# Performance work log

Hardware: AMD Instinct MI355X
Metric: run time of the kernel (lower is better)

The kernel has to match this reference:

```python
import jax, jax.numpy as jnp
import numpy as np

NEG = -1e30  # safe 'log zero' for fp32 (avoids -inf NaNs in grads)


def _ctc_loss(logits, targets, input_lengths, target_lengths):
    """PyTorch-semantics CTC loss: blank=0, reduction='mean', zero_infinity=True.
    logits: [B,T,C] (pre-log-softmax), targets: [B,S] padded, lengths: [B].
    """
    B, T, C = logits.shape
    S = targets.shape[1]
    L = 2 * S + 1  # extended target length (blanks interleaved)
    logp = jax.nn.log_softmax(logits, axis=-1)  # [B,T,C]

    # extended targets: blank, y1, blank, y2, ..., blank
    ext = jnp.zeros((B, L), jnp.int32).at[:, 1::2].set(targets.astype(jnp.int32))
    lp_ext = jnp.take_along_axis(
        logp, jnp.broadcast_to(ext[:, None, :], (B, T, L)), axis=2)  # [B,T,L]

    pos = jnp.arange(L)
    ext_m2 = jnp.pad(ext, ((0, 0), (2, 0)))[:, :L]
    can_skip = (ext != 0) & (ext != ext_m2) & (pos >= 2)  # [B,L]

    def shift(a, k):
        return jnp.pad(a, ((0, 0), (k, 0)), constant_values=NEG)[:, :L]

    def lse3(a, b, c):
        m = jnp.maximum(jnp.maximum(a, b), c)
        return m + jnp.log(jnp.exp(a - m) + jnp.exp(b - m) + jnp.exp(c - m))

    alpha0 = (jnp.full((B, L), NEG, logits.dtype)
              .at[:, 0].set(lp_ext[:, 0, 0])
              .at[:, 1].set(lp_ext[:, 0, 1]))

    def step(alpha, xs):
        lp_t, t = xs  # lp_t: [B,L]
        a2 = shift(alpha, 1)
        a3 = jnp.where(can_skip, shift(alpha, 2), NEG)
        new = lp_t + lse3(alpha, a2, a3)
        # freeze alpha once past each sample's input_length
        alpha = jnp.where((t < input_lengths)[:, None], new, alpha)
        return alpha, None

    lp_T = jnp.swapaxes(lp_ext, 0, 1)  # [T,B,L]
    alpha, _ = jax.lax.scan(step, alpha0, (lp_T[1:], jnp.arange(1, T)))

    i1 = (2 * target_lengths - 1).astype(jnp.int32)
    i2 = (2 * target_lengths).astype(jnp.int32)
    a_last = jnp.take_along_axis(alpha, i1[:, None], axis=1)[:, 0]
    a_blank = jnp.take_along_axis(alpha, i2[:, None], axis=1)[:, 0]
    loss = -jnp.logaddexp(a_last, a_blank)  # [B]
    loss = jnp.where(loss > 1e29, 0.0, loss)  # zero_infinity=True
    return jnp.mean(loss / target_lengths.astype(loss.dtype))


def setup_inputs() -> dict:
    key = jax.random.key(0)
    ks = jax.random.split(key, 8)
    B, T = 32, 2000
    C_err, S_err = 4, 50
    C_ph, S_ph = 64, 200
    error_logits = jax.random.normal(ks[0], (B, T, C_err), jnp.float32)
    phoneme_logits = jax.random.normal(ks[1], (B, T, C_ph), jnp.float32)
    # labels in [1, C): blank=0 never appears in targets
    error_targets = jax.random.randint(ks[2], (B, S_err), 1, C_err, jnp.int32)
    phoneme_targets = jax.random.randint(ks[3], (B, S_ph), 1, C_ph, jnp.int32)
    error_input_lengths = jax.random.randint(ks[4], (B,), T - T // 4, T + 1, jnp.int32)
    phoneme_input_lengths = jax.random.randint(ks[5], (B,), T - T // 4, T + 1, jnp.int32)
    error_target_lengths = jax.random.randint(ks[6], (B,), S_err // 2, S_err + 1, jnp.int32)
    phoneme_target_lengths = jax.random.randint(ks[7], (B,), S_ph // 2, S_ph + 1, jnp.int32)
    return {
        "error_logits": error_logits,
        "phoneme_logits": phoneme_logits,
        "error_targets": error_targets,
        "phoneme_targets": phoneme_targets,
        "error_input_lengths": error_input_lengths,
        "phoneme_input_lengths": phoneme_input_lengths,
        "error_target_lengths": error_target_lengths,
        "phoneme_target_lengths": phoneme_target_lengths,
    }


def reference(error_logits, phoneme_logits, error_targets, phoneme_targets,
              error_input_lengths, phoneme_input_lengths,
              error_target_lengths, phoneme_target_lengths):
    error_weight = 1.0
    phoneme_weight = 1.0
    error_loss = _ctc_loss(error_logits, error_targets,
                           error_input_lengths, error_target_lengths)
    phoneme_loss = _ctc_loss(phoneme_logits, phoneme_targets,
                             phoneme_input_lengths, phoneme_target_lengths)
    total_loss = error_weight * error_loss + phoneme_weight * phoneme_loss
    return total_loss
```

## Files before the change

kernel.cpp:

```cpp
#include <hip/hip_runtime.h>
#include <math.h>


static constexpr float  LOG2E = 1.4426950408889634f;
static constexpr double LN2D  = 0.6931471805599453;
static constexpr int GROWS = 2032;

#define DPP_WAVE_SHL1   0x130
#define DPP_WAVE_SHR1   0x138
#define DPP_ROW_SHR(n)  (0x110 | (n))
#define DPP_ROW_BCAST15 0x142
#define DPP_ROW_BCAST31 0x143

__device__ __forceinline__ float fexp2(float x) {
  return __builtin_amdgcn_exp2f(x);
}
__device__ __forceinline__ float flog2(float x) {
  return __builtin_amdgcn_logf(x);
}

__device__ __forceinline__ double dpp_shr1_f64(double x) {
  int lo = __double2loint(x), hi = __double2hiint(x);
  lo = __builtin_amdgcn_update_dpp(0, lo, DPP_WAVE_SHR1, 0xf, 0xf, true);
  hi = __builtin_amdgcn_update_dpp(0, hi, DPP_WAVE_SHR1, 0xf, 0xf, true);
  return __hiloint2double(hi, lo);
}

__device__ __forceinline__ double dpp_shl1_f64(double x) {
  int lo = __double2loint(x), hi = __double2hiint(x);
  lo = __builtin_amdgcn_update_dpp(0, lo, DPP_WAVE_SHL1, 0xf, 0xf, true);
  hi = __builtin_amdgcn_update_dpp(0, hi, DPP_WAVE_SHL1, 0xf, 0xf, true);
  return __hiloint2double(hi, lo);
}

__device__ __forceinline__ int imax2(int a, int b) { return a > b ? a : b; }

__device__ __forceinline__ int wave_imax(int v) {
  v = imax2(v, __builtin_amdgcn_update_dpp(0, v, DPP_ROW_SHR(1), 0xf, 0xf, true));
  v = imax2(v, __builtin_amdgcn_update_dpp(0, v, DPP_ROW_SHR(2), 0xf, 0xf, true));
  v = imax2(v, __builtin_amdgcn_update_dpp(0, v, DPP_ROW_SHR(4), 0xf, 0xf, true));
  v = imax2(v, __builtin_amdgcn_update_dpp(0, v, DPP_ROW_SHR(8), 0xf, 0xf, true));
  v = imax2(v, __builtin_amdgcn_update_dpp(0, v, DPP_ROW_BCAST15, 0xf, 0xf, true));
  v = imax2(v, __builtin_amdgcn_update_dpp(0, v, DPP_ROW_BCAST31, 0xf, 0xf, true));
  return __builtin_amdgcn_readlane(v, 63);
}


__global__ __launch_bounds__(256) void gather_ph_kernel(
    const float* __restrict__ ph_logits, const float* __restrict__ err_logits,
    const int* __restrict__ ph_tgt,
    float* __restrict__ Gph, float* __restrict__ Lpb_ph,
    float* __restrict__ Lpb_er, float* __restrict__ out) {
  const int bx = blockIdx.x, b = blockIdx.y;
  const int tid = threadIdx.x;
  const int lane = tid & 63, wv = tid >> 6;

  if (bx == 0 && b == 0 && tid == 0) *out = 0.f;

  if (wv == 0 && lane < 32) {
    const int t = bx * 32 + lane;
    if (t < 2000) {
      const float4 v = *(const float4*)(err_logits + ((size_t)b * 2000 + t) * 4);
      const float z0 = v.x * LOG2E;
      const float s = fexp2(z0) + fexp2(v.y * LOG2E) + fexp2(v.z * LOG2E) +
                      fexp2(v.w * LOG2E);
      Lpb_er[(size_t)b * GROWS + t] = z0 - flog2(s);
    }
  }

  const int* tb = ph_tgt + b * 200;
  int idx[4];
  float msk[4];
#pragma unroll
  for (int k = 0; k < 4; ++k) {
    const int si = lane * 4 + k;
    const int cls = (si < 200) ? tb[si] : 0;
    idx[k] = cls << 2;
    msk[k] = (si < 200) ? 1.0f : 0.0f;
  }
  const int t0 = (bx * 4 + wv) * 8;
  float z[8], e[8], s[8];
#pragma unroll
  for (int u = 0; u < 8; ++u) {
    const int t = t0 + u;
    const int tc = (t < 2000) ? t : 1999;
    z[u] = ph_logits[((size_t)b * 2000 + tc) * 64 + lane] * LOG2E;
    e[u] = fexp2(z[u]);
    s[u] = e[u];
  }
#pragma unroll
  for (int off = 32; off >= 1; off >>= 1) {
#pragma unroll
    for (int u = 0; u < 8; ++u) s[u] += __shfl_xor(s[u], off, 64);
  }
#pragma unroll
  for (int u = 0; u < 8; ++u) {
    const int t = t0 + u;
    if (t < 2000) {
      const float e0 = __int_as_float(
          __builtin_amdgcn_readlane(__float_as_int(e[u]), 0));
      const float inv0 = 1.0f / e0;
      float o[4];
#pragma unroll
      for (int k = 0; k < 4; ++k) {
        const float v = __int_as_float(
            __builtin_amdgcn_ds_bpermute(idx[k], __float_as_int(e[u])));
        o[k] = msk[k] * v * inv0;
      }
      *(float4*)(Gph + ((size_t)b * GROWS + t) * 256 + lane * 4) =
          make_float4(o[0], o[1], o[2], o[3]);
      if (lane == 0)
        Lpb_ph[(size_t)b * GROWS + t] = z[u] - flog2(s[u]);
    }
  }
}

template <int P> struct RowP { float v[P]; };

template <int P>
__device__ __forceinline__ void bl_renorm(double (&B)[P], double (&L)[P],
                                          int& K, int tgt) {
  double mm = B[0];
#pragma unroll
  for (int k = 0; k < P; ++k) mm = fmax(fmax(mm, B[k]), L[k]);
  const int ex = (__double2hiint(mm) >> 20) & 0x7ff;
  const int emax = wave_imax(ex);
  if (emax > 0) {
    int d = tgt - emax;
    if (d > 1023) d = 1023;
    if (d < -1022) d = -1022;
    const double sc = __hiloint2double((d + 1023) << 20, 0);
#pragma unroll
    for (int k = 0; k < P; ++k) { B[k] *= sc; L[k] *= sc; }
    K += d;
  }
}

template <int P>
__device__ __forceinline__ void bl_step(double (&B)[P], double (&L)[P],
                                        const double (&skipm)[P],
                                        const RowP<P>& f) {
  const double Lm1 = dpp_shr1_f64(L[P - 1]);
  double nB[P], nL[P];
#pragma unroll
  for (int k = 0; k < P; ++k) {
    const double Lp = (k >= 1) ? L[k - 1] : Lm1;
    nB[k] = B[k] + Lp;
    nL[k] = (double)f.v[k] * fma(skipm[k], Lp, B[k] + L[k]);
  }
#pragma unroll
  for (int k = 0; k < P; ++k) { B[k] = nB[k]; L[k] = nL[k]; }
}

template <int P>
__device__ __forceinline__ void bl_step_bwd(double (&B)[P], double (&L)[P],
                                            const double (&sknext)[P],
                                            const RowP<P>& f) {
  double w[P];
#pragma unroll
  for (int k = 0; k < P; ++k) w[k] = (double)f.v[k] * L[k];
  const double wN = dpp_shl1_f64(w[0]);
  const double BN = dpp_shl1_f64(B[0]);
  double nB[P], nL[P];
#pragma unroll
  for (int k = 0; k < P; ++k) {
    const double wp1 = (k < P - 1) ? w[k + 1] : wN;
    const double Bp1 = (k < P - 1) ? B[k + 1] : BN;
    nB[k] = B[k] + w[k];
    nL[k] = fma(sknext[k], wp1, w[k] + Bp1);
  }
#pragma unroll
  for (int k = 0; k < P; ++k) { B[k] = nB[k]; L[k] = nL[k]; }
}

__device__ __forceinline__ float spb_sum(const float* __restrict__ Lpb,
                                         int len, int lane) {
  float spb = 0.f;
  for (int t0 = lane; t0 < len; t0 += 512) {
#pragma unroll
    for (int u = 0; u < 8; ++u) {
      const int t = t0 + u * 64;
      const int tc = (t < len) ? t : 0;
      const float v = Lpb[tc];
      spb += (t < len) ? v : 0.0f;
    }
  }
#pragma unroll
  for (int off = 32; off >= 1; off >>= 1) spb += __shfl_xor(spb, off, 64);
  return spb;
}

template <int P, typename LdF, typename UseF>
__device__ __forceinline__ void run_fwd(int nsteps, LdF ldrow, UseF use,
                                        double (&B)[P], double (&L)[P],
                                        const double (&sk)[P], int& K) {
  using Buf = decltype(ldrow(1));
  const int ng = nsteps / 16;
  Buf bufA[16], bufB[16];
  if (ng >= 1) {
#pragma unroll
    for (int u = 0; u < 16; ++u) bufA[u] = ldrow(1 + u);
  }
  if (ng >= 2) {
#pragma unroll
    for (int u = 0; u < 16; ++u) bufB[u] = ldrow(17 + u);
  }
  int g = 0;
  for (; g + 2 <= ng; g += 2) {
    bl_renorm<P>(B, L, K, 1523);
    {
      const int gn = (g + 2 < ng) ? (g + 2) : 0;
#pragma unroll
      for (int u = 0; u < 16; ++u) {
        bl_step<P>(B, L, sk, use(bufA[u]));
        bufA[u] = ldrow(1 + gn * 16 + u);
      }
    }
    bl_renorm<P>(B, L, K, 1523);
    {
      const int gn = (g + 3 < ng) ? (g + 3) : 0;
#pragma unroll
      for (int u = 0; u < 16; ++u) {
        bl_step<P>(B, L, sk, use(bufB[u]));
        bufB[u] = ldrow(1 + gn * 16 + u);
      }
    }
  }
  if (g < ng) {
    bl_renorm<P>(B, L, K, 1523);
#pragma unroll
    for (int u = 0; u < 16; ++u) bl_step<P>(B, L, sk, use(bufA[u]));
    ++g;
  }
  {
    const int tstart = 1 + ng * 16;
    Buf bufT[15];
#pragma unroll
    for (int u = 0; u < 15; ++u) {
      int t = tstart + u;
      if (t > nsteps) t = (nsteps > 0) ? nsteps : 1;
      bufT[u] = ldrow(t);
    }
#pragma unroll
    for (int u = 0; u < 15; ++u) {
      if (tstart + u <= nsteps) {
        if (u == 0) bl_renorm<P>(B, L, K, 1523);
        bl_step<P>(B, L, sk, use(bufT[u]));
      }
    }
  }
}

template <int P, typename LdF, typename UseF>
__device__ __forceinline__ void run_bwd(int len, int M, LdF ldrow, UseF use,
                                        double (&B)[P], double (&L)[P],
                                        const double (&sk)[P], int& K) {
  using Buf = decltype(ldrow(1));
  const int ng = M / 16;
  Buf bufA[16], bufB[16];
  if (ng >= 1) {
#pragma unroll
    for (int u = 0; u < 16; ++u) bufA[u] = ldrow(len - 1 - u);
  }
  if (ng >= 2) {
#pragma unroll
    for (int u = 0; u < 16; ++u) bufB[u] = ldrow(len - 17 - u);
  }
  int g = 0;
  for (; g + 2 <= ng; g += 2) {
    bl_renorm<P>(B, L, K, 1023);
    {
      const int jb = (g + 2 < ng) ? (g + 2) * 16 : 0;
#pragma unroll
      for (int u = 0; u < 16; ++u) {
        bl_step_bwd<P>(B, L, sk, use(bufA[u]));
        bufA[u] = ldrow(len - 1 - jb - u);
      }
    }
    bl_renorm<P>(B, L, K, 1023);
    {
      const int jb = (g + 3 < ng) ? (g + 3) * 16 : 0;
#pragma unroll
      for (int u = 0; u < 16; ++u) {
        bl_step_bwd<P>(B, L, sk, use(bufB[u]));
        bufB[u] = ldrow(len - 1 - jb - u);
      }
    }
  }
  if (g < ng) {
    bl_renorm<P>(B, L, K, 1023);
#pragma unroll
    for (int u = 0; u < 16; ++u) bl_step_bwd<P>(B, L, sk, use(bufA[u]));
    ++g;
  }
  {
    const int jstart = ng * 16;
    Buf bufT[15];
#pragma unroll
    for (int u = 0; u < 15; ++u) {
      int j = jstart + u;
      if (j > M - 1) j = (M > 0) ? (M - 1) : 0;
      bufT[u] = ldrow(len - 1 - j);
    }
#pragma unroll
    for (int u = 0; u < 15; ++u) {
      if (jstart + u < M) {
        if (u == 0) bl_renorm<P>(B, L, K, 1023);
        bl_step_bwd<P>(B, L, sk, use(bufT[u]));
      }
    }
  }
}

__global__ __launch_bounds__(64) void ctc_half_kernel(
    const float* __restrict__ Gph, const float* __restrict__ err_logits,
    const int* __restrict__ ph_tgt, const int* __restrict__ err_tgt,
    const int* __restrict__ err_il, const int* __restrict__ ph_il,
    const int* __restrict__ err_tl, const int* __restrict__ ph_tl,
    const float* __restrict__ Lpb_ph, const float* __restrict__ Lpb_er,
    double* __restrict__ st, int* __restrict__ Ks,
    float* __restrict__ spbA) {
  const int blk = blockIdx.x;
  const int dir = blk >> 6;
  const int c = blk & 63;
  const int lane = threadIdx.x;

  double* stB = st + ((size_t)c * 4 + (dir ? 2 : 0)) * 256;
  double* stL = st + ((size_t)c * 4 + (dir ? 3 : 1)) * 256;

  if (c < 32) {
    constexpr int P = 1, S = 50;
    const int* tb = err_tgt + c * 50;
    int len = err_il[c]; if (len > 2000) len = 2000;
    const int tl = err_tl[c];
    const int t_mid = len >> 1;
    const int M = (len - 1) - t_mid;
    const float4* zr = (const float4*)(err_logits + (size_t)c * 2000 * 4);

    const int c1 = tb[(lane < S) ? lane : (S - 1)];
    const float fmask = (lane < S) ? 1.0f : 0.0f;
    auto ldrow = [&](int t) { return zr[t]; };
    auto mkf = [&](const float4& q) {
      RowP<P> f;
      const float zc = (c1 == 1) ? q.y : (c1 == 2) ? q.z : q.w;
      f.v[0] = fmask * fexp2((zc - q.x) * LOG2E);
      return f;
    };

    double B[P], L[P];
    int K = 0;
    if (dir == 0) {
      const float spb = spb_sum(Lpb_er + (size_t)c * GROWS, len, lane);
      double skipm[P];
      skipm[0] =
          (lane >= 1 && lane < S && tb[lane] != tb[lane - 1]) ? 1.0 : 0.0;
      B[0] = 0.0; L[0] = 0.0;
      {
        const float4 q0 = zr[0];
        const int c0 = tb[0];
        const float zc = (c0 == 1) ? q0.y : (c0 == 2) ? q0.z : q0.w;
        if (lane == 0) {
          B[0] = 1.0;
          L[0] = (double)fexp2((zc - q0.x) * LOG2E);
        }
      }
      run_fwd<P>(t_mid, ldrow, mkf, B, L, skipm, K);
      if (lane == 0) spbA[c] = spb;
    } else {
      double sknext[P];
      sknext[0] = (lane + 1 < S && tb[lane + 1] != tb[lane]) ? 1.0 : 0.0;
      B[0] = (lane == tl) ? 1.0 : 0.0;
      L[0] = (lane == tl - 1) ? 1.0 : 0.0;
      run_bwd<P>(len, M, ldrow, mkf, B, L, sknext, K);
    }
    stB[lane] = B[0];
    stL[lane] = L[0];
    if (lane == 0) Ks[dir * 64 + c] = K;
  } else {
    constexpr int P = 4, S = 200, LSTRIDE = 256;
    const int b = c - 32;
    const int* tb = ph_tgt + b * 200;
    int len = ph_il[b]; if (len > 2000) len = 2000;
    const int tl = ph_tl[b];
    const int t_mid = len >> 1;
    const int M = (len - 1) - t_mid;
    const float* Glab = Gph + (size_t)b * GROWS * 256;
    const float* gp = Glab + lane * P;

    auto ldrow = [&](int t) {
      RowP<P> r;
      const float4 a = *(const float4*)(gp + (size_t)t * LSTRIDE);
      r.v[0] = a.x; r.v[1] = a.y; r.v[2] = a.z; r.v[3] = a.w;
      return r;
    };
    auto use_id = [](const RowP<P>& r) { return r; };

    double B[P], L[P];
    int K = 0;
    if (dir == 0) {
      const float spb = spb_sum(Lpb_ph + (size_t)b * GROWS, len, lane);
      double skipm[P];
#pragma unroll
      for (int k = 0; k < P; ++k) {
        const int s = lane * P + k;
        skipm[k] = (s >= 1 && s < S && tb[s] != tb[s - 1]) ? 1.0 : 0.0;
      }
#pragma unroll
      for (int k = 0; k < P; ++k) { B[k] = 0.0; L[k] = 0.0; }
      {
        const float r0 = Glab[0];
        if (lane == 0) { B[0] = 1.0; L[0] = (double)r0; }
      }
      run_fwd<P>(t_mid, ldrow, use_id, B, L, skipm, K);
      if (lane == 0) spbA[c] = spb;
    } else {
      double sknext[P];
#pragma unroll
      for (int k = 0; k < P; ++k) {
        const int s = lane * P + k;
        sknext[k] = (s + 1 < S && tb[s + 1] != tb[s]) ? 1.0 : 0.0;
      }
#pragma unroll
      for (int k = 0; k < P; ++k) {
        const int s = lane * P + k;
        B[k] = (s == tl) ? 1.0 : 0.0;
        L[k] = (s == tl - 1) ? 1.0 : 0.0;
      }
      run_bwd<P>(len, M, ldrow, use_id, B, L, sknext, K);
    }
#pragma unroll
    for (int k = 0; k < P; ++k) {
      stB[lane * P + k] = B[k];
      stL[lane * P + k] = L[k];
    }
    if (lane == 0) Ks[dir * 64 + c] = K;
  }
}

__global__ __launch_bounds__(64) void ctc_merge_kernel(
    const double* __restrict__ st, const int* __restrict__ Ks,
    const float* __restrict__ spbA, const int* __restrict__ err_tl,
    const int* __restrict__ ph_tl, float* __restrict__ out) {
  const int c = blockIdx.x;
  const int lane = threadIdx.x;
  const double* Bf = st + ((size_t)c * 4 + 0) * 256;
  const double* Lf = st + ((size_t)c * 4 + 1) * 256;
  const double* Bb = st + ((size_t)c * 4 + 2) * 256;
  const double* Lb = st + ((size_t)c * 4 + 3) * 256;
  double dot;
  if (c < 32) {
    dot = Bf[lane] * Bb[lane] + Lf[lane] * Lb[lane];
  } else {
    dot = 0.0;
#pragma unroll
    for (int k = 0; k < 4; ++k) {
      const int i = lane * 4 + k;
      dot += Bf[i] * Bb[i] + Lf[i] * Lb[i];
    }
  }
#pragma unroll
  for (int off = 32; off >= 1; off >>= 1) dot += __shfl_xor(dot, off, 64);
  if (lane == 0) {
    const int K2 = Ks[c] + Ks[64 + c];
    const int tl = (c < 32) ? err_tl[c] : ph_tl[c - 32];
    float loss =
        (float)((double)K2 * LN2D - log(dot) - (double)spbA[c] * LN2D);
    if (!(loss < 1e29f)) loss = 0.f;
    atomicAdd(out, loss / ((float)tl * 32.0f));
  }
}


__global__ __launch_bounds__(256) void softmax4_kernel(
    const float* __restrict__ x, float* __restrict__ p, int nrows) {
  int r = blockIdx.x * blockDim.x + threadIdx.x;
  if (r >= nrows) return;
  float4 v = *reinterpret_cast<const float4*>(x + (size_t)r * 4);
  float z0 = v.x * LOG2E, z1 = v.y * LOG2E, z2 = v.z * LOG2E, z3 = v.w * LOG2E;
  float m = fmaxf(fmaxf(z0, z1), fmaxf(z2, z3));
  float e0 = fexp2(z0 - m), e1 = fexp2(z1 - m);
  float e2 = fexp2(z2 - m), e3 = fexp2(z3 - m);
  float inv = 1.0f / (e0 + e1 + e2 + e3);
  float4 o;
  o.x = e0 * inv; o.y = e1 * inv; o.z = e2 * inv; o.w = e3 * inv;
  *reinterpret_cast<float4*>(p + (size_t)r * 4) = o;
}

__global__ __launch_bounds__(256) void softmax64_kernel(
    const float* __restrict__ x, float* __restrict__ p, int nrows) {
  int row = blockIdx.x * 4 + (threadIdx.x >> 6);
  int lane = threadIdx.x & 63;
  if (row >= nrows) return;
  float z = x[(size_t)row * 64 + lane] * LOG2E;
  float m = z;
#pragma unroll
  for (int off = 32; off >= 1; off >>= 1) m = fmaxf(m, __shfl_xor(m, off, 64));
  float e = fexp2(z - m);
  float s = e;
#pragma unroll
  for (int off = 32; off >= 1; off >>= 1) s += __shfl_xor(s, off, 64);
  p[(size_t)row * 64 + lane] = e * (1.0f / s);
}

template <int C, int S, int R>
__device__ __forceinline__ void ctc_chain_lin_fb(
    const float* __restrict__ p_b, const int* __restrict__ tgt_b,
    int len, int tl, float* __restrict__ out, double* sa) {
  constexpr int L = 2 * S + 1;
  const int lane = threadIdx.x;
  int idx[R];
  double skipm[R];
#pragma unroll
  for (int j = 0; j < R; ++j) {
    const int l = lane * R + j;
    int cls = 0;
    bool sk = false;
    if (l & 1) {
      const int s = (l - 1) >> 1;
      const int sc = (s < S) ? s : (S - 1);
      cls = tgt_b[sc];
      if (s >= 1 && s < S) sk = (cls != tgt_b[s - 1]);
    }
    idx[j] = cls * 4;
    skipm[j] = sk ? 1.0 : 0.0;
  }
  double alpha[R];
#pragma unroll
  for (int j = 0; j < R; ++j) {
    const int l = lane * R + j;
    alpha[j] = (l <= 1) ? (double)p_b[idx[j] >> 2] : 0.0;
  }
  int K = 0;
  const int cl = lane & (C - 1);
  float rv = p_b[(size_t)((1 < len - 1) ? 1 : (len - 1)) * C + cl];
  float pf[R];
#pragma unroll
  for (int j = 0; j < R; ++j)
    pf[j] = __int_as_float(__builtin_amdgcn_ds_bpermute(idx[j], __float_as_int(rv)));
  rv = p_b[(size_t)((2 < len - 1) ? 2 : (len - 1)) * C + cl];
  for (int t = 1; t < len; ++t) {
    if ((t & 31) == 0) {
      double m = alpha[0];
#pragma unroll
      for (int j = 1; j < R; ++j) m = fmax(m, alpha[j]);
#pragma unroll
      for (int off = 1; off < 64; off <<= 1) m = fmax(m, __shfl_xor(m, off, 64));
      const long long bits = __double_as_longlong(m);
      const int e = (int)((bits >> 52) & 0x7FF);
      if (e > 0) {
        const double sc = __longlong_as_double((long long)(2046 - e) << 52);
#pragma unroll
        for (int j = 0; j < R; ++j) alpha[j] *= sc;
        K += 1023 - e;
      }
    }
    const int tn = (t + 2 < len) ? (t + 2) : (len - 1);
    const float rvn = p_b[(size_t)tn * C + cl];
    float pfn[R];
#pragma unroll
    for (int j = 0; j < R; ++j)
      pfn[j] = __int_as_float(__builtin_amdgcn_ds_bpermute(idx[j], __float_as_int(rv)));
    double am1 = __shfl_up(alpha[R - 1], 1, 64);
    double am2 = __shfl_up(alpha[R - 2], 1, 64);
    if (lane == 0) { am1 = 0.0; am2 = 0.0; }
    double na[R];
#pragma unroll
    for (int j = 0; j < R; ++j) {
      const double a0 = alpha[j];
      const double a1 = (j >= 1) ? alpha[j - 1] : am1;
      const double a2 = (j >= 2) ? alpha[j - 2] : ((j == 1) ? am1 : am2);
      double s = a0 + a1;
      s = fma(skipm[j], a2, s);
      na[j] = (double)pf[j] * s;
    }
#pragma unroll
    for (int j = 0; j < R; ++j) alpha[j] = na[j];
#pragma unroll
    for (int j = 0; j < R; ++j) pf[j] = pfn[j];
    rv = rvn;
  }
#pragma unroll
  for (int j = 0; j < R; ++j) {
    const int l = lane * R + j;
    if (l < L) sa[l] = alpha[j];
  }
  __syncthreads();
  if (lane == 0) {
    const double a = sa[2 * tl - 1] + sa[2 * tl];
    float loss = (float)((double)K * LN2D - log(a));
    if (!(loss < 1e29f)) loss = 0.0f;
    atomicAdd(out, loss / ((float)tl * 32.0f));
  }
}

__global__ __launch_bounds__(64) void ctc_chains_fb_kernel(
    const float* __restrict__ p_err, const float* __restrict__ p_ph,
    const int* __restrict__ err_tgt, const int* __restrict__ ph_tgt,
    const int* __restrict__ err_il, const int* __restrict__ ph_il,
    const int* __restrict__ err_tl, const int* __restrict__ ph_tl,
    float* __restrict__ out) {
  __shared__ double sa[512];
  const int T = 2000;
  const int blk = blockIdx.x;
  if (blk < 32) {
    const int b = blk;
    int len = err_il[b]; if (len > T) len = T;
    ctc_chain_lin_fb<4, 50, 2>(p_err + (size_t)b * T * 4, err_tgt + b * 50, len,
                               err_tl[b], out, sa);
  } else {
    const int b = blk - 32;
    int len = ph_il[b]; if (len > T) len = T;
    ctc_chain_lin_fb<64, 200, 7>(p_ph + (size_t)b * T * 64, ph_tgt + b * 200,
                                 len, ph_tl[b], out, sa);
  }
}


extern "C" void kernel_launch(void* const* d_in, const int* in_sizes, int n_in,
                              void* d_out, int out_size, void* d_ws,
                              size_t ws_size, hipStream_t stream) {
  const float* err_logits = (const float*)d_in[0];
  const float* ph_logits  = (const float*)d_in[1];
  const int* err_tgt = (const int*)d_in[2];
  const int* ph_tgt  = (const int*)d_in[3];
  const int* err_il  = (const int*)d_in[4];
  const int* ph_il   = (const int*)d_in[5];
  const int* err_tl  = (const int*)d_in[6];
  const int* ph_tl   = (const int*)d_in[7];
  float* out = (float*)d_out;

  const size_t gph = (size_t)32 * GROWS * 256;
  const size_t lpb = (size_t)32 * GROWS;
  const size_t nst = (size_t)64 * 4 * 256;
  const size_t need =
      (gph + 2 * lpb) * sizeof(float) + nst * sizeof(double) + 256 * 4;

  if (ws_size >= need) {
    float* Gph = (float*)d_ws;
    float* Lpb_ph = Gph + gph;
    float* Lpb_er = Lpb_ph + lpb;
    double* st = (double*)(Lpb_er + lpb);
    int* Ks = (int*)(st + nst);
    float* spbA = (float*)(Ks + 128);
    gather_ph_kernel<<<dim3(63, 32), 256, 0, stream>>>(
        ph_logits, err_logits, ph_tgt, Gph, Lpb_ph, Lpb_er, out);
    ctc_half_kernel<<<128, 64, 0, stream>>>(
        Gph, err_logits, ph_tgt, err_tgt, err_il, ph_il, err_tl, ph_tl,
        Lpb_ph, Lpb_er, st, Ks, spbA);
    ctc_merge_kernel<<<64, 64, 0, stream>>>(st, Ks, spbA, err_tl, ph_tl, out);
  } else {
    (void)hipMemsetAsync(d_out, 0, sizeof(float), stream);
    const int B = 32, T = 2000;
    const int rows = B * T;
    float* p_err = (float*)d_ws;
    float* p_ph  = p_err + (size_t)rows * 4;
    softmax4_kernel<<<(rows + 255) / 256, 256, 0, stream>>>(err_logits, p_err, rows);
    softmax64_kernel<<<(rows + 3) / 4, 256, 0, stream>>>(ph_logits, p_ph, rows);
    ctc_chains_fb_kernel<<<64, 64, 0, stream>>>(p_err, p_ph, err_tgt, ph_tgt,
                                                err_il, ph_il, err_tl, ph_tl, out);
  }
}
```

Before: 202.2 us.

## Run error CTC as full forward pass in one block, drop its bidirectional split

The small error-CTC chains (S=50) now run the whole forward recursion in a single wave and compute the loss directly via shared memory, instead of splitting into forward and backward halves merged in a separate kernel. The phoneme chains keep the forward/backward split, and the merge kernel now handles only those 32 phoneme samples. The prefetch depth for the error chain drops from 16 to 8 rows. The error chain's serial length doubles, so its blocks run about twice as long as before. It is meant to finish within the phoneme halves' critical path while cutting block count and merge work.

```diff
diff --git a/kernel.cpp b/kernel.cpp
--- a/kernel.cpp
+++ b/kernel.cpp
@@ -45,6 +45,12 @@
   return __builtin_amdgcn_readlane(v, 63);
 }
 
+__device__ __forceinline__ void wait_lgkm0() {
+  __builtin_amdgcn_sched_barrier(0);
+  __builtin_amdgcn_s_waitcnt(49279);
+  __builtin_amdgcn_sched_barrier(0);
+}
+
 
 __global__ __launch_bounds__(256) void gather_ph_kernel(
     const float* __restrict__ ph_logits, const float* __restrict__ err_logits,
@@ -117,6 +123,13 @@
 
 template <int P> struct RowP { float v[P]; };
 
+__device__ __forceinline__ RowP<4> ld4(const float* p) {
+  RowP<4> r;
+  const float4 a = *(const float4*)p;
+  r.v[0] = a.x; r.v[1] = a.y; r.v[2] = a.z; r.v[3] = a.w;
+  return r;
+}
+
 template <int P>
 __device__ __forceinline__ void bl_renorm(double (&B)[P], double (&L)[P],
                                           int& K, int tgt) {
@@ -190,281 +203,338 @@
   return spb;
 }
 
-template <int P, typename LdF, typename UseF>
-__device__ __forceinline__ void run_fwd(int nsteps, LdF ldrow, UseF use,
-                                        double (&B)[P], double (&L)[P],
-                                        const double (&sk)[P], int& K) {
-  using Buf = decltype(ldrow(1));
-  const int ng = nsteps / 16;
-  Buf bufA[16], bufB[16];
-  if (ng >= 1) {
-#pragma unroll
-    for (int u = 0; u < 16; ++u) bufA[u] = ldrow(1 + u);
-  }
-  if (ng >= 2) {
-#pragma unroll
-    for (int u = 0; u < 16; ++u) bufB[u] = ldrow(17 + u);
-  }
-  int g = 0;
-  for (; g + 2 <= ng; g += 2) {
-    bl_renorm<P>(B, L, K, 1523);
-    {
-      const int gn = (g + 2 < ng) ? (g + 2) : 0;
-#pragma unroll
-      for (int u = 0; u < 16; ++u) {
-        bl_step<P>(B, L, sk, use(bufA[u]));
-        bufA[u] = ldrow(1 + gn * 16 + u);
-      }
-    }
-    bl_renorm<P>(B, L, K, 1523);
-    {
-      const int gn = (g + 3 < ng) ? (g + 3) : 0;
-#pragma unroll
-      for (int u = 0; u < 16; ++u) {
-        bl_step<P>(B, L, sk, use(bufB[u]));
-        bufB[u] = ldrow(1 + gn * 16 + u);
-      }
-    }
-  }
-  if (g < ng) {
-    bl_renorm<P>(B, L, K, 1523);
-#pragma unroll
-    for (int u = 0; u < 16; ++u) bl_step<P>(B, L, sk, use(bufA[u]));
-    ++g;
-  }
-  {
-    const int tstart = 1 + ng * 16;
-    Buf bufT[15];
-#pragma unroll
-    for (int u = 0; u < 15; ++u) {
-      int t = tstart + u;
-      if (t > nsteps) t = (nsteps > 0) ? nsteps : 1;
-      bufT[u] = ldrow(t);
-    }
-#pragma unroll
-    for (int u = 0; u < 15; ++u) {
-      if (tstart + u <= nsteps) {
-        if (u == 0) bl_renorm<P>(B, L, K, 1523);
-        bl_step<P>(B, L, sk, use(bufT[u]));
-      }
-    }
-  }
-}
-
-template <int P, typename LdF, typename UseF>
-__device__ __forceinline__ void run_bwd(int len, int M, LdF ldrow, UseF use,
-                                        double (&B)[P], double (&L)[P],
-                                        const double (&sk)[P], int& K) {
-  using Buf = decltype(ldrow(1));
-  const int ng = M / 16;
-  Buf bufA[16], bufB[16];
-  if (ng >= 1) {
-#pragma unroll
-    for (int u = 0; u < 16; ++u) bufA[u] = ldrow(len - 1 - u);
-  }
-  if (ng >= 2) {
-#pragma unroll
-    for (int u = 0; u < 16; ++u) bufB[u] = ldrow(len - 17 - u);
-  }
-  int g = 0;
-  for (; g + 2 <= ng; g += 2) {
-    bl_renorm<P>(B, L, K, 1023);
-    {
-      const int jb = (g + 2 < ng) ? (g + 2) * 16 : 0;
-#pragma unroll
-      for (int u = 0; u < 16; ++u) {
-        bl_step_bwd<P>(B, L, sk, use(bufA[u]));
-        bufA[u] = ldrow(len - 1 - jb - u);
-      }
-    }
-    bl_renorm<P>(B, L, K, 1023);
-    {
-      const int jb = (g + 3 < ng) ? (g + 3) * 16 : 0;
-#pragma unroll
-      for (int u = 0; u < 16; ++u) {
-        bl_step_bwd<P>(B, L, sk, use(bufB[u]));
-        bufB[u] = ldrow(len - 1 - jb - u);
-      }
-    }
-  }
-  if (g < ng) {
-    bl_renorm<P>(B, L, K, 1023);
-#pragma unroll
-    for (int u = 0; u < 16; ++u) bl_step_bwd<P>(B, L, sk, use(bufA[u]));
-    ++g;
-  }
-  {
-    const int jstart = ng * 16;
-    Buf bufT[15];
-#pragma unroll
-    for (int u = 0; u < 15; ++u) {
-      int j = jstart + u;
-      if (j > M - 1) j = (M > 0) ? (M - 1) : 0;
-      bufT[u] = ldrow(len - 1 - j);
-    }
-#pragma unroll
-    for (int u = 0; u < 15; ++u) {
-      if (jstart + u < M) {
-        if (u == 0) bl_renorm<P>(B, L, K, 1023);
-        bl_step_bwd<P>(B, L, sk, use(bufT[u]));
-      }
-    }
-  }
-}
-
-__global__ __launch_bounds__(64) void ctc_half_kernel(
+__global__ __launch_bounds__(64) void ctc_main_kernel(
     const float* __restrict__ Gph, const float* __restrict__ err_logits,
     const int* __restrict__ ph_tgt, const int* __restrict__ err_tgt,
     const int* __restrict__ err_il, const int* __restrict__ ph_il,
     const int* __restrict__ err_tl, const int* __restrict__ ph_tl,
     const float* __restrict__ Lpb_ph, const float* __restrict__ Lpb_er,
-    double* __restrict__ st, int* __restrict__ Ks,
-    float* __restrict__ spbA) {
+    double* __restrict__ st, int* __restrict__ Ks, float* __restrict__ spbA,
+    float* __restrict__ out) {
+  __shared__ double sa[128];
   const int blk = blockIdx.x;
-  const int dir = blk >> 6;
-  const int c = blk & 63;
   const int lane = threadIdx.x;
 
-  double* stB = st + ((size_t)c * 4 + (dir ? 2 : 0)) * 256;
-  double* stL = st + ((size_t)c * 4 + (dir ? 3 : 1)) * 256;
-
-  if (c < 32) {
-    constexpr int P = 1, S = 50;
+  if (blk < 32) {
+    constexpr int S = 50;
+    const int c = blk;
     const int* tb = err_tgt + c * 50;
     int len = err_il[c]; if (len > 2000) len = 2000;
     const int tl = err_tl[c];
-    const int t_mid = len >> 1;
-    const int M = (len - 1) - t_mid;
     const float4* zr = (const float4*)(err_logits + (size_t)c * 2000 * 4);
 
+    const float spb = spb_sum(Lpb_er + (size_t)c * GROWS, len, lane);
     const int c1 = tb[(lane < S) ? lane : (S - 1)];
     const float fmask = (lane < S) ? 1.0f : 0.0f;
-    auto ldrow = [&](int t) { return zr[t]; };
-    auto mkf = [&](const float4& q) {
-      RowP<P> f;
-      const float zc = (c1 == 1) ? q.y : (c1 == 2) ? q.z : q.w;
-      f.v[0] = fmask * fexp2((zc - q.x) * LOG2E);
-      return f;
-    };
-
-    double B[P], L[P];
+    double skipm[1];
+    skipm[0] = (lane >= 1 && lane < S && tb[lane] != tb[lane - 1]) ? 1.0 : 0.0;
+
+    double B[1], L[1];
+    B[0] = 0.0; L[0] = 0.0;
+    {
+      const float4 q0 = zr[0];
+      const int c0 = tb[0];
+      const float zc = (c0 == 1) ? q0.y : (c0 == 2) ? q0.z : q0.w;
+      if (lane == 0) {
+        B[0] = 1.0;
+        L[0] = (double)fexp2((zc - q0.x) * LOG2E);
+      }
+    }
     int K = 0;
-    if (dir == 0) {
-      const float spb = spb_sum(Lpb_er + (size_t)c * GROWS, len, lane);
-      double skipm[P];
-      skipm[0] =
-          (lane >= 1 && lane < S && tb[lane] != tb[lane - 1]) ? 1.0 : 0.0;
-      B[0] = 0.0; L[0] = 0.0;
+
+    const int nsteps = len - 1;
+    const int ng = nsteps / 8;
+    float4 bufA[8], bufB[8];
+    if (ng >= 1) {
+#pragma unroll
+      for (int u = 0; u < 8; ++u) bufA[u] = zr[1 + u];
+    }
+    if (ng >= 2) {
+#pragma unroll
+      for (int u = 0; u < 8; ++u) bufB[u] = zr[9 + u];
+    }
+    int g = 0;
+    for (; g + 2 <= ng; g += 2) {
+      bl_renorm<1>(B, L, K, 1523);
       {
-        const float4 q0 = zr[0];
-        const int c0 = tb[0];
-        const float zc = (c0 == 1) ? q0.y : (c0 == 2) ? q0.z : q0.w;
-        if (lane == 0) {
-          B[0] = 1.0;
-          L[0] = (double)fexp2((zc - q0.x) * LOG2E);
-        }
-      }
-      run_fwd<P>(t_mid, ldrow, mkf, B, L, skipm, K);
-      if (lane == 0) spbA[c] = spb;
-    } else {
-      double sknext[P];
-      sknext[0] = (lane + 1 < S && tb[lane + 1] != tb[lane]) ? 1.0 : 0.0;
-      B[0] = (lane == tl) ? 1.0 : 0.0;
-      L[0] = (lane == tl - 1) ? 1.0 : 0.0;
-      run_bwd<P>(len, M, ldrow, mkf, B, L, sknext, K);
-    }
-    stB[lane] = B[0];
-    stL[lane] = L[0];
-    if (lane == 0) Ks[dir * 64 + c] = K;
-  } else {
-    constexpr int P = 4, S = 200, LSTRIDE = 256;
-    const int b = c - 32;
-    const int* tb = ph_tgt + b * 200;
-    int len = ph_il[b]; if (len > 2000) len = 2000;
-    const int tl = ph_tl[b];
-    const int t_mid = len >> 1;
-    const int M = (len - 1) - t_mid;
-    const float* Glab = Gph + (size_t)b * GROWS * 256;
-    const float* gp = Glab + lane * P;
-
-    auto ldrow = [&](int t) {
-      RowP<P> r;
-      const float4 a = *(const float4*)(gp + (size_t)t * LSTRIDE);
-      r.v[0] = a.x; r.v[1] = a.y; r.v[2] = a.z; r.v[3] = a.w;
-      return r;
-    };
-    auto use_id = [](const RowP<P>& r) { return r; };
-
-    double B[P], L[P];
-    int K = 0;
-    if (dir == 0) {
-      const float spb = spb_sum(Lpb_ph + (size_t)b * GROWS, len, lane);
-      double skipm[P];
-#pragma unroll
-      for (int k = 0; k < P; ++k) {
-        const int s = lane * P + k;
-        skipm[k] = (s >= 1 && s < S && tb[s] != tb[s - 1]) ? 1.0 : 0.0;
-      }
-#pragma unroll
-      for (int k = 0; k < P; ++k) { B[k] = 0.0; L[k] = 0.0; }
+        const int gn = (g + 2 < ng) ? (g + 2) : 0;
+        const float4* nx = zr + 1 + gn * 8;
+#pragma unroll
+        for (int u = 0; u < 8; ++u) {
+          RowP<1> f;
+          const float4 q = bufA[u];
+          const float zc = (c1 == 1) ? q.y : (c1 == 2) ? q.z : q.w;
+          f.v[0] = fmask * fexp2((zc - q.x) * LOG2E);
+          bl_step<1>(B, L, skipm, f);
+          bufA[u] = nx[u];
+        }
+      }
+      bl_renorm<1>(B, L, K, 1523);
       {
-        const float r0 = Glab[0];
-        if (lane == 0) { B[0] = 1.0; L[0] = (double)r0; }
-      }
-      run_fwd<P>(t_mid, ldrow, use_id, B, L, skipm, K);
-      if (lane == 0) spbA[c] = spb;
-    } else {
-      double sknext[P];
-#pragma unroll
-      for (int k = 0; k < P; ++k) {
-        const int s = lane * P + k;
-        sknext[k] = (s + 1 < S && tb[s + 1] != tb[s]) ? 1.0 : 0.0;
-      }
-#pragma unroll
-      for (int k = 0; k < P; ++k) {
-        const int s = lane * P + k;
-        B[k] = (s == tl) ? 1.0 : 0.0;
-        L[k] = (s == tl - 1) ? 1.0 : 0.0;
-      }
-      run_bwd<P>(len, M, ldrow, use_id, B, L, sknext, K);
-    }
+        const int gn = (g + 3 < ng) ? (g + 3) : 0;
+        const float4* nx = zr + 1 + gn * 8;
+#pragma unroll
+        for (int u = 0; u < 8; ++u) {
+          RowP<1> f;
+          const float4 q = bufB[u];
+          const float zc = (c1 == 1) ? q.y : (c1 == 2) ? q.z : q.w;
+          f.v[0] = fmask * fexp2((zc - q.x) * LOG2E);
+          bl_step<1>(B, L, skipm, f);
+          bufB[u] = nx[u];
+        }
+      }
+    }
+    if (g < ng) {
+      bl_renorm<1>(B, L, K, 1523);
+#pragma unroll
+      for (int u = 0; u < 8; ++u) {
+        RowP<1> f;
+        const float4 q = bufA[u];
+        const float zc = (c1 == 1) ? q.y : (c1 == 2) ? q.z : q.w;
+        f.v[0] = fmask * fexp2((zc - q.x) * LOG2E);
+        bl_step<1>(B, L, skipm, f);
+      }
+      ++g;
+    }
+    {
+      const int tstart = 1 + ng * 8;
+      float4 bufT[7];
+#pragma unroll
+      for (int u = 0; u < 7; ++u) {
+        int t = tstart + u;
+        if (t > nsteps) t = (nsteps > 0) ? nsteps : 1;
+        bufT[u] = zr[t];
+      }
+#pragma unroll
+      for (int u = 0; u < 7; ++u) {
+        if (tstart + u <= nsteps) {
+          if (u == 0) bl_renorm<1>(B, L, K, 1523);
+          RowP<1> f;
+          const float4 q = bufT[u];
+          const float zc = (c1 == 1) ? q.y : (c1 == 2) ? q.z : q.w;
+          f.v[0] = fmask * fexp2((zc - q.x) * LOG2E);
+          bl_step<1>(B, L, skipm, f);
+        }
+      }
+    }
+
+    double* saB = sa;
+    double* saL = sa + 64;
+    saB[lane] = B[0];
+    saL[lane] = L[0];
+    wait_lgkm0();
+    if (lane == 0) {
+      const double a = saL[tl - 1] + saB[tl];
+      float loss = (float)((double)K * LN2D - log(a) - (double)spb * LN2D);
+      if (!(loss < 1e29f)) loss = 0.f;
+      atomicAdd(out, loss / ((float)tl * 32.0f));
+    }
+    return;
+  }
+
+  constexpr int P = 4, S = 200, LSTRIDE = 256;
+  const int dir = (blk >= 64) ? 1 : 0;
+  const int b = blk - (dir ? 64 : 32);
+  const int* tb = ph_tgt + b * 200;
+  int len = ph_il[b]; if (len > 2000) len = 2000;
+  const int tl = ph_tl[b];
+  const int t_mid = len >> 1;
+  const float* Glab = Gph + (size_t)b * GROWS * 256;
+  const float* gp = Glab + lane * P;
+
+  double B[P], L[P];
+  int K = 0;
+
+  if (dir == 0) {
+    const float spb = spb_sum(Lpb_ph + (size_t)b * GROWS, len, lane);
+    double skipm[P];
+#pragma unroll
+    for (int k = 0; k < P; ++k) {
+      const int s = lane * P + k;
+      skipm[k] = (s >= 1 && s < S && tb[s] != tb[s - 1]) ? 1.0 : 0.0;
+    }
+#pragma unroll
+    for (int k = 0; k < P; ++k) { B[k] = 0.0; L[k] = 0.0; }
+    {
+      const float r0 = Glab[0];
+      if (lane == 0) { B[0] = 1.0; L[0] = (double)r0; }
+    }
+
+    const int nsteps = t_mid;
+    const int ngroups = nsteps / 16;
+    RowP<P> bufA[16], bufB[16];
+    if (ngroups >= 1) {
+      const float* rb = gp + (size_t)1 * LSTRIDE;
+#pragma unroll
+      for (int u = 0; u < 16; ++u) bufA[u] = ld4(rb + (size_t)u * LSTRIDE);
+    }
+    if (ngroups >= 2) {
+      const float* rb = gp + (size_t)17 * LSTRIDE;
+#pragma unroll
+      for (int u = 0; u < 16; ++u) bufB[u] = ld4(rb + (size_t)u * LSTRIDE);
+    }
+    int g = 0;
+    for (; g + 2 <= ngroups; g += 2) {
+      {
+        bl_renorm<P>(B, L, K, 1523);
+        const int gn = (g + 2 < ngroups) ? (g + 2) : 0;
+        const float* nx = gp + (size_t)(1 + gn * 16) * LSTRIDE;
+#pragma unroll
+        for (int u = 0; u < 16; ++u) {
+          bl_step<P>(B, L, skipm, bufA[u]);
+          bufA[u] = ld4(nx + (size_t)u * LSTRIDE);
+        }
+      }
+      {
+        bl_renorm<P>(B, L, K, 1523);
+        const int gn = (g + 3 < ngroups) ? (g + 3) : 0;
+        const float* nx = gp + (size_t)(1 + gn * 16) * LSTRIDE;
+#pragma unroll
+        for (int u = 0; u < 16; ++u) {
+          bl_step<P>(B, L, skipm, bufB[u]);
+          bufB[u] = ld4(nx + (size_t)u * LSTRIDE);
+        }
+      }
+    }
+    if (g < ngroups) {
+      bl_renorm<P>(B, L, K, 1523);
+#pragma unroll
+      for (int u = 0; u < 16; ++u) bl_step<P>(B, L, skipm, bufA[u]);
+      ++g;
+    }
+    {
+      const int tstart = 1 + ngroups * 16;
+      RowP<P> bufT[15];
+#pragma unroll
+      for (int u = 0; u < 15; ++u) {
+        int t = tstart + u;
+        if (t > nsteps) t = (nsteps > 0) ? nsteps : 1;
+        bufT[u] = ld4(gp + (size_t)t * LSTRIDE);
+      }
+#pragma unroll
+      for (int u = 0; u < 15; ++u) {
+        if (tstart + u <= nsteps) {
+          if (u == 0) bl_renorm<P>(B, L, K, 1523);
+          bl_step<P>(B, L, skipm, bufT[u]);
+        }
+      }
+    }
+    if (lane == 0) { Ks[b] = 0; spbA[b] = spb; }
+    double* stB = st + ((size_t)b * 4 + 0) * 256;
+    double* stL = st + ((size_t)b * 4 + 1) * 256;
 #pragma unroll
     for (int k = 0; k < P; ++k) {
       stB[lane * P + k] = B[k];
       stL[lane * P + k] = L[k];
     }
-    if (lane == 0) Ks[dir * 64 + c] = K;
+    if (lane == 0) Ks[b] = K;
+  } else {
+    double sknext[P];
+#pragma unroll
+    for (int k = 0; k < P; ++k) {
+      const int s = lane * P + k;
+      sknext[k] = (s + 1 < S && tb[s + 1] != tb[s]) ? 1.0 : 0.0;
+    }
+#pragma unroll
+    for (int k = 0; k < P; ++k) {
+      const int s = lane * P + k;
+      B[k] = (s == tl) ? 1.0 : 0.0;
+      L[k] = (s == tl - 1) ? 1.0 : 0.0;
+    }
+
+    const int M = (len - 1) - t_mid;
+    const int ngroups = M / 16;
+    RowP<P> bufA[16], bufB[16];
+    if (ngroups >= 1) {
+      const float* rb = gp + (size_t)(len - 1) * LSTRIDE;
+#pragma unroll
+      for (int u = 0; u < 16; ++u) bufA[u] = ld4(rb - u * LSTRIDE);
+    }
+    if (ngroups >= 2) {
+      const float* rb = gp + (size_t)(len - 17) * LSTRIDE;
+#pragma unroll
+      for (int u = 0; u < 16; ++u) bufB[u] = ld4(rb - u * LSTRIDE);
+    }
+    int g = 0;
+    for (; g + 2 <= ngroups; g += 2) {
+      {
+        bl_renorm<P>(B, L, K, 1023);
+        const int jb = (g + 2 < ngroups) ? (g + 2) * 16 : 0;
+        const float* nx = gp + (size_t)(len - 1 - jb) * LSTRIDE;
+#pragma unroll
+        for (int u = 0; u < 16; ++u) {
+          bl_step_bwd<P>(B, L, sknext, bufA[u]);
+          bufA[u] = ld4(nx - u * LSTRIDE);
+        }
+      }
+      {
+        bl_renorm<P>(B, L, K, 1023);
+        const int jb = (g + 3 < ngroups) ? (g + 3) * 16 : 0;
+        const float* nx = gp + (size_t)(len - 1 - jb) * LSTRIDE;
+#pragma unroll
+        for (int u = 0; u < 16; ++u) {
+          bl_step_bwd<P>(B, L, sknext, bufB[u]);
+          bufB[u] = ld4(nx - u * LSTRIDE);
+        }
+      }
+    }
+    if (g < ngroups) {
+      bl_renorm<P>(B, L, K, 1023);
+#pragma unroll
+      for (int u = 0; u < 16; ++u) bl_step_bwd<P>(B, L, sknext, bufA[u]);
+      ++g;
+    }
+    {
+      const int jstart = ngroups * 16;
+      RowP<P> bufT[15];
+#pragma unroll
+      for (int u = 0; u < 15; ++u) {
+        int j = jstart + u;
+        if (j > M - 1) j = (M > 0) ? (M - 1) : 0;
+        bufT[u] = ld4(gp + (size_t)(len - 1 - j) * LSTRIDE);
+      }
+#pragma unroll
+      for (int u = 0; u < 15; ++u) {
+        if (jstart + u < M) {
+          if (u == 0) bl_renorm<P>(B, L, K, 1023);
+          bl_step_bwd<P>(B, L, sknext, bufT[u]);
+        }
+      }
+    }
+    double* stB = st + ((size_t)b * 4 + 2) * 256;
+    double* stL = st + ((size_t)b * 4 + 3) * 256;
+#pragma unroll
+    for (int k = 0; k < P; ++k) {
+      stB[lane * P + k] = B[k];
+      stL[lane * P + k] = L[k];
+    }
+    if (lane == 0) Ks[32 + b] = K;
   }
 }
 
 __global__ __launch_bounds__(64) void ctc_merge_kernel(
     const double* __restrict__ st, const int* __restrict__ Ks,
-    const float* __restrict__ spbA, const int* __restrict__ err_tl,
-    const int* __restrict__ ph_tl, float* __restrict__ out) {
-  const int c = blockIdx.x;
+    const float* __restrict__ spbA, const int* __restrict__ ph_tl,
+    float* __restrict__ out) {
+  const int b = blockIdx.x;
   const int lane = threadIdx.x;
-  const double* Bf = st + ((size_t)c * 4 + 0) * 256;
-  const double* Lf = st + ((size_t)c * 4 + 1) * 256;
-  const double* Bb = st + ((size_t)c * 4 + 2) * 256;
-  const double* Lb = st + ((size_t)c * 4 + 3) * 256;
-  double dot;
-  if (c < 32) {
-    dot = Bf[lane] * Bb[lane] + Lf[lane] * Lb[lane];
-  } else {
-    dot = 0.0;
-#pragma unroll
-    for (int k = 0; k < 4; ++k) {
-      const int i = lane * 4 + k;
-      dot += Bf[i] * Bb[i] + Lf[i] * Lb[i];
-    }
+  const double* Bf = st + ((size_t)b * 4 + 0) * 256;
+  const double* Lf = st + ((size_t)b * 4 + 1) * 256;
+  const double* Bb = st + ((size_t)b * 4 + 2) * 256;
+  const double* Lb = st + ((size_t)b * 4 + 3) * 256;
+  double dot = 0.0;
+#pragma unroll
+  for (int k = 0; k < 4; ++k) {
+    const int i = lane * 4 + k;
+    dot += Bf[i] * Bb[i] + Lf[i] * Lb[i];
   }
 #pragma unroll
   for (int off = 32; off >= 1; off >>= 1) dot += __shfl_xor(dot, off, 64);
   if (lane == 0) {
-    const int K2 = Ks[c] + Ks[64 + c];
-    const int tl = (c < 32) ? err_tl[c] : ph_tl[c - 32];
+    const int K2 = Ks[b] + Ks[32 + b];
+    const int tl = ph_tl[b];
     float loss =
-        (float)((double)K2 * LN2D - log(dot) - (double)spbA[c] * LN2D);
+        (float)((double)K2 * LN2D - log(dot) - (double)spbA[b] * LN2D);
     if (!(loss < 1e29f)) loss = 0.f;
     atomicAdd(out, loss / ((float)tl * 32.0f));
   }
@@ -631,9 +701,9 @@
 
   const size_t gph = (size_t)32 * GROWS * 256;
   const size_t lpb = (size_t)32 * GROWS;
-  const size_t nst = (size_t)64 * 4 * 256;
+  const size_t nst = (size_t)32 * 4 * 256;
   const size_t need =
-      (gph + 2 * lpb) * sizeof(float) + nst * sizeof(double) + 256 * 4;
+      (gph + 2 * lpb) * sizeof(float) + nst * sizeof(double) + 128 * 4;
 
   if (ws_size >= need) {
     float* Gph = (float*)d_ws;
@@ -641,13 +711,13 @@
     float* Lpb_er = Lpb_ph + lpb;
     double* st = (double*)(Lpb_er + lpb);
     int* Ks = (int*)(st + nst);
-    float* spbA = (float*)(Ks + 128);
+    float* spbA = (float*)(Ks + 64);
     gather_ph_kernel<<<dim3(63, 32), 256, 0, stream>>>(
         ph_logits, err_logits, ph_tgt, Gph, Lpb_ph, Lpb_er, out);
-    ctc_half_kernel<<<128, 64, 0, stream>>>(
+    ctc_main_kernel<<<96, 64, 0, stream>>>(
         Gph, err_logits, ph_tgt, err_tgt, err_il, ph_il, err_tl, ph_tl,
-        Lpb_ph, Lpb_er, st, Ks, spbA);
-    ctc_merge_kernel<<<64, 64, 0, stream>>>(st, Ks, spbA, err_tl, ph_tl, out);
+        Lpb_ph, Lpb_er, st, Ks, spbA, out);
+    ctc_merge_kernel<<<32, 64, 0, stream>>>(st, Ks, spbA, ph_tl, out);
   } else {
     (void)hipMemsetAsync(d_out, 0, sizeof(float), stream);
     const int B = 32, T = 2000;
```

After: 207.2 us. +2.5%, slower.
